# Kernel optimization log

Hardware: AMD Instinct MI355X
Metric: run time of the kernel (lower is better)

The kernel has to match this reference:

```python
import jax, jax.numpy as jnp
import numpy as np

H = 32

def setup_inputs() -> dict:
    key = jax.random.key(0)
    ks = jax.random.split(key, 8)
    B, S = 256, 4096
    scale = 1.0 / np.sqrt(H)
    return {
        "lstm_outputs": jax.random.normal(ks[0], (B, S, H), dtype=jnp.float32),
        "final_hidden": jax.random.normal(ks[1], (B, H), dtype=jnp.float32),
        "Wq": jax.random.uniform(ks[2], (H, H), jnp.float32, -scale, scale),
        "bq": jax.random.uniform(ks[3], (H,), jnp.float32, -scale, scale),
        "Wk": jax.random.uniform(ks[4], (H, H), jnp.float32, -scale, scale),
        "bk": jax.random.uniform(ks[5], (H,), jnp.float32, -scale, scale),
        "Wv": jax.random.uniform(ks[6], (H, 1), jnp.float32, -scale, scale),
        "bv": jax.random.uniform(ks[7], (1,), jnp.float32, -scale, scale),
    }

def reference(lstm_outputs, final_hidden, Wq, bq, Wk, bk, Wv, bv):
    # keys: [B,S,H], query: [B,H]
    keys = jnp.einsum('bsh,hd->bsd', lstm_outputs, Wk) + bk
    query = final_hidden @ Wq + bq
    tanhed = jnp.tanh(query[:, None, :] + keys)            # [B,S,H]
    scores = jnp.einsum('bsh,h->bs', tanhed, Wv[:, 0]) + bv[0]  # [B,S]
    att_weights = jax.nn.softmax(scores, axis=-1)          # [B,S]
    context = jnp.einsum('bs,bsh->bh', att_weights, keys)  # [B,H]
    return context, att_weights
```

## Files before the change

kernel.cpp:

```cpp
#include <hip/hip_runtime.h>
#include <math.h>

#define HD 32
#define BB 256
#define SS 4096
#define BLK 256
#define POSB 256
#define NCH (SS / POSB)
#define PADW 40
#define PSTRIDE 33

typedef short bf16x8 __attribute__((ext_vector_type(8)));
typedef float f32x4 __attribute__((ext_vector_type(4)));

__device__ __forceinline__ float tanh_fast(float x) {
  float e = __builtin_amdgcn_exp2f(x * 2.8853900817779268f);
  return 1.0f - 2.0f * __builtin_amdgcn_rcpf(e + 1.0f);
}
__device__ __forceinline__ float exp_fast(float x) {
  return __builtin_amdgcn_exp2f(x * 1.4426950408889634f);
}
__device__ __forceinline__ short bf16_trunc(float x) {
  return (short)(__float_as_uint(x) >> 16);
}
__device__ __forceinline__ float hi_part(float x) {
  return __uint_as_float(__float_as_uint(x) & 0xffff0000u);
}

__global__ void __launch_bounds__(BLK, 4) bahdanau_p1(
    const float* __restrict__ lstm, const float* __restrict__ fh,
    const float* __restrict__ Wq, const float* __restrict__ bq,
    const float* __restrict__ Wk, const float* __restrict__ bk,
    const float* __restrict__ Wv, const float* __restrict__ bv,
    float* __restrict__ scores_out, float* __restrict__ partials) {
  __shared__ short sWkTh[HD * PADW];
  __shared__ short sWkTl[HD * PADW];
  __shared__ float sQB[HD];
  __shared__ float sWv[HD];
  __shared__ float sYp[4][HD];
  __shared__ float sRedL[4];

  const int tid = threadIdx.x;
  const int b = blockIdx.x >> 4;
  const int chunk = blockIdx.x & (NCH - 1);
  const int base = chunk * POSB;
  const int lane = tid & 63, w = tid >> 6;
  const int col = lane & 15, quad = lane >> 4;

  const float* gx = lstm + ((size_t)b * SS + base + w * 64) * HD;
  const float* rp = gx + (size_t)col * HD + quad * 8;
  float4 xa0 = ((const float4*)(rp + 0 * 16 * HD))[0];
  float4 xb0 = ((const float4*)(rp + 0 * 16 * HD))[1];
  float4 xa1 = ((const float4*)(rp + 1 * 16 * HD))[0];
  float4 xb1 = ((const float4*)(rp + 1 * 16 * HD))[1];
  float4 xa2 = ((const float4*)(rp + 2 * 16 * HD))[0];
  float4 xb2 = ((const float4*)(rp + 2 * 16 * HD))[1];
  float4 xa3 = ((const float4*)(rp + 3 * 16 * HD))[0];
  float4 xb3 = ((const float4*)(rp + 3 * 16 * HD))[1];

  {
    float4 w4 = ((const float4*)Wk)[tid];
    const int k = tid >> 3, h0 = (tid & 7) * 4;
    const float v[4] = {w4.x, w4.y, w4.z, w4.w};
#pragma unroll
    for (int i = 0; i < 4; i++) {
      const float hf = hi_part(v[i]);
      sWkTh[(h0 + i) * PADW + k] = bf16_trunc(v[i]);
      sWkTl[(h0 + i) * PADW + k] = bf16_trunc(v[i] - hf);
    }
  }
  if (tid < HD) {
    float acc = bq[tid] + bk[tid];
    const float* fhb = fh + b * HD;
#pragma unroll
    for (int j = 0; j < HD; j++) acc += fhb[j] * Wq[j * HD + tid];
    sQB[tid] = acc;
    sWv[tid] = Wv[tid];
  }
  __syncthreads();

  bf16x8 Bh0 = *(const bf16x8*)&sWkTh[(col) * PADW + quad * 8];
  bf16x8 Bl0 = *(const bf16x8*)&sWkTl[(col) * PADW + quad * 8];
  bf16x8 Bh1 = *(const bf16x8*)&sWkTh[(16 + col) * PADW + quad * 8];
  bf16x8 Bl1 = *(const bf16x8*)&sWkTl[(16 + col) * PADW + quad * 8];
  const float qb0 = sQB[col], qb1 = sQB[16 + col];
  const float wv0 = sWv[col], wv1 = sWv[16 + col];
  const float bv0 = bv[0];

  float lAcc = 0.f;
  float yp[8];
#pragma unroll
  for (int j = 0; j < 8; j++) yp[j] = 0.f;

#define MT_STEP(mt, XA, XB)                                                    \
  {                                                                            \
    const float xs[8] = {XA.x, XA.y, XA.z, XA.w, XB.x, XB.y, XB.z, XB.w};      \
    bf16x8 Ah, Al;                                                             \
    _Pragma("unroll") for (int j = 0; j < 8; j++) {                            \
      const float hf = hi_part(xs[j]);                                         \
      Ah[j] = bf16_trunc(xs[j]);                                               \
      Al[j] = bf16_trunc(xs[j] - hf);                                          \
    }                                                                          \
    f32x4 c0 = {0.f, 0.f, 0.f, 0.f}, c1 = {0.f, 0.f, 0.f, 0.f};                \
    c0 = __builtin_amdgcn_mfma_f32_16x16x32_bf16(Ah, Bh0, c0, 0, 0, 0);        \
    c1 = __builtin_amdgcn_mfma_f32_16x16x32_bf16(Ah, Bh1, c1, 0, 0, 0);        \
    c0 = __builtin_amdgcn_mfma_f32_16x16x32_bf16(Al, Bh0, c0, 0, 0, 0);        \
    c1 = __builtin_amdgcn_mfma_f32_16x16x32_bf16(Al, Bh1, c1, 0, 0, 0);        \
    c0 = __builtin_amdgcn_mfma_f32_16x16x32_bf16(Ah, Bl0, c0, 0, 0, 0);        \
    c1 = __builtin_amdgcn_mfma_f32_16x16x32_bf16(Ah, Bl1, c1, 0, 0, 0);        \
    float esc[4];                                                              \
    _Pragma("unroll") for (int r = 0; r < 4; r++) {                            \
      float t = tanh_fast(qb0 + c0[r]) * wv0 + tanh_fast(qb1 + c1[r]) * wv1;   \
      t += __shfl_xor(t, 1, 64);                                               \
      t += __shfl_xor(t, 2, 64);                                               \
      t += __shfl_xor(t, 4, 64);                                               \
      t += __shfl_xor(t, 8, 64);                                               \
      esc[r] = exp_fast(t + bv0);                                              \
    }                                                                          \
    const int srcLane = (col >> 2) * 16;                                       \
    const float g0 = __shfl(esc[0], srcLane, 64);                              \
    const float g1 = __shfl(esc[1], srcLane, 64);                              \
    const float g2 = __shfl(esc[2], srcLane, 64);                              \
    const float g3 = __shfl(esc[3], srcLane, 64);                              \
    const int rr = col & 3;                                                    \
    const float e_m = (rr == 0) ? g0 : (rr == 1) ? g1 : (rr == 2) ? g2 : g3;   \
    if (lane < 16)                                                             \
      scores_out[(size_t)b * SS + base + w * 64 + mt * 16 + lane] = e_m;       \
    lAcc += (lane < 16) ? e_m : 0.f;                                           \
    _Pragma("unroll") for (int j = 0; j < 8; j++)                              \
        yp[j] = fmaf(e_m, xs[j], yp[j]);                                       \
  }

  MT_STEP(0, xa0, xb0)
  MT_STEP(1, xa1, xb1)
  MT_STEP(2, xa2, xb2)
  MT_STEP(3, xa3, xb3)
#undef MT_STEP

#pragma unroll
  for (int j = 0; j < 8; j++) {
    yp[j] += __shfl_xor(yp[j], 1, 64);
    yp[j] += __shfl_xor(yp[j], 2, 64);
    yp[j] += __shfl_xor(yp[j], 4, 64);
    yp[j] += __shfl_xor(yp[j], 8, 64);
  }
  if (col == 0) {
#pragma unroll
    for (int j = 0; j < 8; j++) sYp[w][quad * 8 + j] = yp[j];
  }
#pragma unroll
  for (int off = 32; off >= 1; off >>= 1) lAcc += __shfl_xor(lAcc, off, 64);
  if (lane == 0) sRedL[w] = lAcc;
  __syncthreads();

  if (tid < HD) {
    float y = sYp[0][tid] + sYp[1][tid] + sYp[2][tid] + sYp[3][tid];
    float* p = partials + (size_t)blockIdx.x * PSTRIDE;
    p[1 + tid] = y;
    if (tid == 0) p[0] = sRedL[0] + sRedL[1] + sRedL[2] + sRedL[3];
  }
}

__global__ void __launch_bounds__(BLK) bahdanau_p2(
    const float* __restrict__ partials, const float* __restrict__ Wk,
    const float* __restrict__ bk, float* __restrict__ ctx_out,
    float* __restrict__ scores) {
  const int blk = blockIdx.x;
  const int b = blk >> 2;
  const int tid = threadIdx.x;
  __shared__ float sY[HD];

  float L = 0.f;
#pragma unroll
  for (int c = 0; c < NCH; c++)
    L += partials[(size_t)(b * NCH + c) * PSTRIDE];
  const float invL = __builtin_amdgcn_rcpf(L);

  if ((blk & 3) == 0) {
    if (tid < HD) {
      float y = 0.f;
#pragma unroll
      for (int c = 0; c < NCH; c++)
        y += partials[(size_t)(b * NCH + c) * PSTRIDE + 1 + tid];
      sY[tid] = y;
    }
    __syncthreads();
    if (tid < HD) {
      float c = bk[tid] * L;
#pragma unroll
      for (int j = 0; j < HD; j++) c = fmaf(sY[j], Wk[j * HD + tid], c);
      ctx_out[b * HD + tid] = c * invL;
    }
  }

  float4* srow = (float4*)(scores + (size_t)b * SS + (blk & 3) * 1024);
  float4 s = srow[tid];
  s.x *= invL; s.y *= invL; s.z *= invL; s.w *= invL;
  srow[tid] = s;
}

extern "C" void kernel_launch(void* const* d_in, const int* in_sizes, int n_in,
                              void* d_out, int out_size, void* d_ws,
                              size_t ws_size, hipStream_t stream) {
  const float* lstm = (const float*)d_in[0];
  const float* fh   = (const float*)d_in[1];
  const float* Wq   = (const float*)d_in[2];
  const float* bq   = (const float*)d_in[3];
  const float* Wk   = (const float*)d_in[4];
  const float* bk   = (const float*)d_in[5];
  const float* Wv   = (const float*)d_in[6];
  const float* bv   = (const float*)d_in[7];

  float* out = (float*)d_out;
  float* ctx_out = out;
  float* scores = out + BB * HD;
  float* partials = (float*)d_ws;

  bahdanau_p1<<<BB * NCH, BLK, 0, stream>>>(lstm, fh, Wq, bq, Wk, bk, Wv, bv,
                                            scores, partials);
  bahdanau_p2<<<BB * 4, BLK, 0, stream>>>(partials, Wk, bk, ctx_out, scores);
}
```

Measured before the change: 206.8 us.

## Process four chunks per block with double-buffered register prefetch of inputs

Each phase-1 block now handles four consecutive 256-position chunks instead of one, which cuts the grid by four. It prefetches the next chunk's lstm rows into a second register buffer while the current chunk runs through MFMA, tanh and exp. This amortises the per-block setup (Wk split into shared memory, query projection) and hides global load latency behind compute. The cost is more live registers and less parallelism, which may reduce occupancy, and phase 2 now reduces fewer partial records per batch row.

```diff
diff --git a/kernel.cpp b/kernel.cpp
--- a/kernel.cpp
+++ b/kernel.cpp
@@ -7,6 +7,8 @@
 #define BLK 256
 #define POSB 256
 #define NCH (SS / POSB)
+#define GRP 4
+#define NREC (NCH / GRP)
 #define PADW 40
 #define PSTRIDE 33
 
@@ -41,22 +43,25 @@
   __shared__ float sRedL[4];
 
   const int tid = threadIdx.x;
-  const int b = blockIdx.x >> 4;
-  const int chunk = blockIdx.x & (NCH - 1);
-  const int base = chunk * POSB;
+  const int b = blockIdx.x >> 2;
+  const int grp = blockIdx.x & (NREC - 1);
+  const int base = grp * (GRP * POSB);
   const int lane = tid & 63, w = tid >> 6;
   const int col = lane & 15, quad = lane >> 4;
 
-  const float* gx = lstm + ((size_t)b * SS + base + w * 64) * HD;
-  const float* rp = gx + (size_t)col * HD + quad * 8;
-  float4 xa0 = ((const float4*)(rp + 0 * 16 * HD))[0];
-  float4 xb0 = ((const float4*)(rp + 0 * 16 * HD))[1];
-  float4 xa1 = ((const float4*)(rp + 1 * 16 * HD))[0];
-  float4 xb1 = ((const float4*)(rp + 1 * 16 * HD))[1];
-  float4 xa2 = ((const float4*)(rp + 2 * 16 * HD))[0];
-  float4 xb2 = ((const float4*)(rp + 2 * 16 * HD))[1];
-  float4 xa3 = ((const float4*)(rp + 3 * 16 * HD))[0];
-  float4 xb3 = ((const float4*)(rp + 3 * 16 * HD))[1];
+  const float* wp =
+      lstm + ((size_t)b * SS + base + w * 64 + col) * HD + quad * 8;
+
+  float4 xa[2][4], xb[2][4];
+#define LOADP(bufi, cc, mt)                                                    \
+  {                                                                            \
+    const float* p_ = wp + (size_t)(cc) * (POSB * HD) + (mt) * (16 * HD);      \
+    xa[bufi][mt] = ((const float4*)p_)[0];                                     \
+    xb[bufi][mt] = ((const float4*)p_)[1];                                     \
+  }
+
+#pragma unroll
+  for (int mt = 0; mt < 4; mt++) LOADP(0, 0, mt)
 
   {
     float4 w4 = ((const float4*)Wk)[tid];
@@ -79,8 +84,8 @@
   }
   __syncthreads();
 
-  bf16x8 Bh0 = *(const bf16x8*)&sWkTh[(col) * PADW + quad * 8];
-  bf16x8 Bl0 = *(const bf16x8*)&sWkTl[(col) * PADW + quad * 8];
+  bf16x8 Bh0 = *(const bf16x8*)&sWkTh[(col)*PADW + quad * 8];
+  bf16x8 Bl0 = *(const bf16x8*)&sWkTl[(col)*PADW + quad * 8];
   bf16x8 Bh1 = *(const bf16x8*)&sWkTh[(16 + col) * PADW + quad * 8];
   bf16x8 Bl1 = *(const bf16x8*)&sWkTl[(16 + col) * PADW + quad * 8];
   const float qb0 = sQB[col], qb1 = sQB[16 + col];
@@ -92,7 +97,9 @@
 #pragma unroll
   for (int j = 0; j < 8; j++) yp[j] = 0.f;
 
-#define MT_STEP(mt, XA, XB)                                                    \
+  const size_t srow = (size_t)b * SS + base;
+
+#define MT_STEP(posoff, XA, XB)                                                \
   {                                                                            \
     const float xs[8] = {XA.x, XA.y, XA.z, XA.w, XB.x, XB.y, XB.z, XB.w};      \
     bf16x8 Ah, Al;                                                             \
@@ -124,18 +131,27 @@
     const float g3 = __shfl(esc[3], srcLane, 64);                              \
     const int rr = col & 3;                                                    \
     const float e_m = (rr == 0) ? g0 : (rr == 1) ? g1 : (rr == 2) ? g2 : g3;   \
-    if (lane < 16)                                                             \
-      scores_out[(size_t)b * SS + base + w * 64 + mt * 16 + lane] = e_m;       \
+    if (lane < 16) scores_out[srow + (posoff) + lane] = e_m;                   \
     lAcc += (lane < 16) ? e_m : 0.f;                                           \
     _Pragma("unroll") for (int j = 0; j < 8; j++)                              \
         yp[j] = fmaf(e_m, xs[j], yp[j]);                                       \
   }
 
-  MT_STEP(0, xa0, xb0)
-  MT_STEP(1, xa1, xb1)
-  MT_STEP(2, xa2, xb2)
-  MT_STEP(3, xa3, xb3)
+#pragma unroll 1
+  for (int cc2 = 0; cc2 < GRP; cc2 += 2) {
+#pragma unroll
+    for (int mt = 0; mt < 4; mt++) {
+      LOADP(1, cc2 + 1, mt)
+      MT_STEP(cc2 * POSB + w * 64 + mt * 16, xa[0][mt], xb[0][mt])
+    }
+#pragma unroll
+    for (int mt = 0; mt < 4; mt++) {
+      if (cc2 + 2 < GRP) LOADP(0, cc2 + 2, mt)
+      MT_STEP((cc2 + 1) * POSB + w * 64 + mt * 16, xa[1][mt], xb[1][mt])
+    }
+  }
 #undef MT_STEP
+#undef LOADP
 
 #pragma unroll
   for (int j = 0; j < 8; j++) {
@@ -172,24 +188,24 @@
 
   float L = 0.f;
 #pragma unroll
-  for (int c = 0; c < NCH; c++)
-    L += partials[(size_t)(b * NCH + c) * PSTRIDE];
+  for (int c = 0; c < NREC; c++)
+    L += partials[(size_t)(b * NREC + c) * PSTRIDE];
   const float invL = __builtin_amdgcn_rcpf(L);
 
   if ((blk & 3) == 0) {
     if (tid < HD) {
       float y = 0.f;
 #pragma unroll
-      for (int c = 0; c < NCH; c++)
-        y += partials[(size_t)(b * NCH + c) * PSTRIDE + 1 + tid];
+      for (int c = 0; c < NREC; c++)
+        y += partials[(size_t)(b * NREC + c) * PSTRIDE + 1 + tid];
       sY[tid] = y;
     }
     __syncthreads();
     if (tid < HD) {
-      float c = bk[tid] * L;
-#pragma unroll
-      for (int j = 0; j < HD; j++) c = fmaf(sY[j], Wk[j * HD + tid], c);
-      ctx_out[b * HD + tid] = c * invL;
+      float cv = bk[tid] * L;
+#pragma unroll
+      for (int j = 0; j < HD; j++) cv = fmaf(sY[j], Wk[j * HD + tid], cv);
+      ctx_out[b * HD + tid] = cv * invL;
     }
   }
 
@@ -216,7 +232,7 @@
   float* scores = out + BB * HD;
   float* partials = (float*)d_ws;
 
-  bahdanau_p1<<<BB * NCH, BLK, 0, stream>>>(lstm, fh, Wq, bq, Wk, bk, Wv, bv,
-                                            scores, partials);
+  bahdanau_p1<<<BB * NREC, BLK, 0, stream>>>(lstm, fh, Wq, bq, Wk, bk, Wv, bv,
+                                             scores, partials);
   bahdanau_p2<<<BB * 4, BLK, 0, stream>>>(partials, Wk, bk, ctx_out, scores);
 }
```

Measured after the change: 255.9 us. 1.24x slower.
